# Kernel optimization log

Hardware: AMD Instinct MI355X
Metric: run time of the kernel (lower is better)

Reference implementation:

```python
import jax, jax.numpy as jnp
import numpy as np

B, T, D, SD, CHUNK = 4, 4096, 1024, 512, 32


def setup_inputs() -> dict:
    key = jax.random.key(0)
    ks = jax.random.split(key, 6)
    sc_in = 1.0 / np.sqrt(D)
    sc_out = 1.0 / np.sqrt(2 * SD)
    return {
        "x": jax.random.normal(ks[0], (B, T, D), jnp.float32),
        "Wt": jax.random.normal(ks[1], (D, SD), jnp.float32) * sc_in,
        "bt": jnp.zeros((SD,), jnp.float32),
        "Wr": jax.random.normal(ks[2], (D, SD), jnp.float32) * sc_in,
        "br": jnp.zeros((SD,), jnp.float32),
        "Wi": jax.random.normal(ks[3], (D, 2 * SD), jnp.float32) * sc_in,
        "bi": jnp.zeros((2 * SD,), jnp.float32),
        "Wo": jax.random.normal(ks[4], (2 * SD, D), jnp.float32) * sc_out,
        "bo": jnp.zeros((D,), jnp.float32),
        "gamma": jnp.ones((D,), jnp.float32),
        "beta": jnp.zeros((D,), jnp.float32),
    }


def _rotation_scan(theta, retain, b_r, b_i, chunk):
    # theta/retain/b_*: [B, T, d]. Chunked linear recurrence h[t]=a[t]*h[t-1]+b[t]
    # with a[t] = retain[t]*e^{i theta[t]}, done in log-magnitude/angle space.
    Bsz, Tlen, d = theta.shape
    K = min(chunk, Tlen)
    n = Tlen // K  # T assumed divisible by K (4096 / 32)
    resh = lambda a: a.reshape(Bsz, n, K, d).transpose(1, 0, 2, 3)  # [n,B,K,d]
    th_c, rt_c, br_c, bi_c = resh(theta), resh(retain), resh(b_r), resh(b_i)

    def step(carry, xs):
        h_r, h_i = carry  # [B, d]
        th, rt, cb_r, cb_i = xs  # [B, K, d]
        cum_log_mag = jnp.cumsum(jnp.log(jnp.clip(rt, 1e-6, None)), axis=1)
        cum_mag = jnp.exp(cum_log_mag)
        cum_th = jnp.cumsum(th, axis=1)
        cum_cos = jnp.cos(cum_th)
        cum_sin = jnp.sin(cum_th)
        cum_a_r = cum_mag * cum_cos
        cum_a_i = cum_mag * cum_sin
        inv_mag = 1.0 / jnp.clip(cum_mag, 1e-8, None)
        inv_r = inv_mag * cum_cos          # cos(-t) = cos(t)
        inv_i = -inv_mag * cum_sin         # sin(-t) = -sin(t)
        scaled_b_r = inv_r * cb_r - inv_i * cb_i
        scaled_b_i = inv_r * cb_i + inv_i * cb_r
        cum_b_r = jnp.cumsum(scaled_b_r, axis=1)
        cum_b_i = jnp.cumsum(scaled_b_i, axis=1)
        tot_r = h_r[:, None] + cum_b_r
        tot_i = h_i[:, None] + cum_b_i
        ch_r = cum_a_r * tot_r - cum_a_i * tot_i
        ch_i = cum_a_r * tot_i + cum_a_i * tot_r
        return (ch_r[:, -1], ch_i[:, -1]), (ch_r, ch_i)

    h0 = (jnp.zeros((Bsz, d), theta.dtype), jnp.zeros((Bsz, d), theta.dtype))
    _, (out_r, out_i) = jax.lax.scan(step, h0, (th_c, rt_c, br_c, bi_c))
    back = lambda a: a.transpose(1, 0, 2, 3).reshape(Bsz, Tlen, d)
    return back(out_r), back(out_i)


def reference(x, Wt, bt, Wr, br, Wi, bi, Wo, bo, gamma, beta):
    d = Wt.shape[1]
    theta = x @ Wt + bt                       # [B,T,d]
    retain = jax.nn.sigmoid(x @ Wr + br)      # [B,T,d]
    inp = x @ Wi + bi                          # [B,T,2d]
    inp_r, inp_i = inp[..., :d], inp[..., d:]
    drive = 1.0 - retain
    out_r, out_i = _rotation_scan(theta, retain, drive * inp_r, drive * inp_i, CHUNK)
    out = jnp.concatenate([out_r, out_i], axis=-1)  # [B,T,2d]
    y = x + out @ Wo + bo
    mu = jnp.mean(y, axis=-1, keepdims=True)
    var = jnp.var(y, axis=-1, keepdims=True)
    return (y - mu) / jnp.sqrt(var + 1e-5) * gamma + beta
```

## Files before the change

kernel.cpp:

```cpp
#include <hip/hip_runtime.h>
#include <cstdint>


typedef __bf16 bf16x8 __attribute__((ext_vector_type(8)));
typedef float  f32x4  __attribute__((ext_vector_type(4)));

#define AS1 __attribute__((address_space(1)))
#define AS3 __attribute__((address_space(3)))

__device__ __forceinline__ void gload16(const void* g, void* l) {
  __builtin_amdgcn_global_load_lds((const AS1 void*)g, (AS3 void*)l, 16, 0, 0);
}

__device__ __forceinline__ ushort f2bf(float f) {
  union { float f; uint32_t u; } v; v.f = f;
  uint32_t u = v.u;
  uint32_t r = u + 0x7FFFu + ((u >> 16) & 1u);
  return (ushort)(r >> 16);
}
__device__ __forceinline__ float bf2f(ushort u) {
  union { uint32_t x; float f; } v; v.x = (uint32_t)u << 16; return v.f;
}
__device__ __forceinline__ void st_f(float* p, size_t i, float v)  { p[i] = v; }
__device__ __forceinline__ void st_f(ushort* p, size_t i, float v) { p[i] = f2bf(v); }

__global__ __launch_bounds__(256) void tconv(const float* __restrict__ src, int R, int C,
                                             ushort* __restrict__ dst, int row_off) {
  __shared__ float tile[32][33];
  int tx = threadIdx.x, ty = threadIdx.y;
  int rb = blockIdx.y * 32, cb = blockIdx.x * 32;
#pragma unroll
  for (int yy = 0; yy < 4; ++yy) {
    int r = rb + ty + yy * 8;
    tile[ty + yy * 8][tx] = src[(size_t)r * C + cb + tx];
  }
  __syncthreads();
#pragma unroll
  for (int yy = 0; yy < 4; ++yy) {
    int c = cb + ty + yy * 8;
    dst[(size_t)(row_off + c) * R + rb + tx] = f2bf(tile[tx][ty + yy * 8]);
  }
}

__global__ __launch_bounds__(256) void pack_bias(const float* __restrict__ bt,
                                                 const float* __restrict__ br,
                                                 const float* __restrict__ bi,
                                                 float* __restrict__ bcat) {
  int i = blockIdx.x * 256 + threadIdx.x;
  bcat[i] = (i < 512) ? bt[i] : (i < 1024 ? br[i - 512] : bi[i - 1024]);
}

__global__ __launch_bounds__(256) void xconv(const float4* __restrict__ src,
                                             ushort* __restrict__ dst, int n4) {
  int i = blockIdx.x * 256 + threadIdx.x;
  if (i < n4) {
    float4 v = src[i];
    ushort4 o;
    o.x = f2bf(v.x); o.y = f2bf(v.y); o.z = f2bf(v.z); o.w = f2bf(v.w);
    *(ushort4*)(dst + (size_t)i * 4) = o;
  }
}

template <typename CT>
__global__ __launch_bounds__(512, 2) void gemm256(const ushort* __restrict__ A,
                                                  const ushort* __restrict__ Bt,
                                                  CT* __restrict__ C,
                                                  const float* __restrict__ bias,
                                                  int M, int N, int K, int nbn) {
  __shared__ alignas(16) ushort As[2][256 * 64];
  __shared__ alignas(16) ushort Bs[2][256 * 64];

  const int cpx = gridDim.x >> 3;
  const int wg = ((int)blockIdx.x & 7) * cpx + ((int)blockIdx.x >> 3);
  const int bm = wg / nbn, bn = wg % nbn;

  const int t = threadIdx.x;
  const int l = t & 63, w = t >> 6;
  const int wm = w >> 2, wn = w & 3;
  const int r = l & 15, kq = l >> 4;

  const size_t a0 = (size_t)bm * 256 * K;
  const size_t b0 = (size_t)bn * 256 * K;

  const int srow = t >> 3;
  const int sslot = (t & 7) ^ (srow & 7);
  const ushort* gA = A + a0 + (size_t)srow * K + sslot * 8;
  const ushort* gB = Bt + b0 + (size_t)srow * K + sslot * 8;
  const int lboff = w * 1024 + l * 16;

  f32x4 acc[8][4] = {};
  const int NKT = K >> 6;

#define STG(G, LB, kt, u) \
  gload16((G) + (size_t)((u) * 64) * K + (size_t)(kt) * 64, (char*)(LB) + (u) * 8192 + lboff)

#define QUAD(ph)                                                               \
  do {                                                                         \
    bf16x8 aF[2][2];                                                           \
    _Pragma("unroll")                                                          \
    for (int ii = 0; ii < 2; ++ii) {                                           \
      const int row = wm * 128 + ((ph) * 2 + ii) * 16 + r;                     \
      _Pragma("unroll")                                                        \
      for (int ks = 0; ks < 2; ++ks) {                                         \
        const int j = (ks * 4 + kq) ^ (r & 7);                                 \
        aF[ii][ks] = *(const bf16x8*)&As[cur][row * 64 + j * 8];               \
      }                                                                        \
    }                                                                          \
    __builtin_amdgcn_s_setprio(1);                                             \
    _Pragma("unroll")                                                          \
    for (int ii = 0; ii < 2; ++ii)                                             \
      _Pragma("unroll")                                                        \
      for (int jn = 0; jn < 4; ++jn)                                           \
        _Pragma("unroll")                                                      \
        for (int ks = 0; ks < 2; ++ks)                                         \
          acc[(ph) * 2 + ii][jn] = __builtin_amdgcn_mfma_f32_16x16x32_bf16(    \
              aF[ii][ks], bF[jn][ks], acc[(ph) * 2 + ii][jn], 0, 0, 0);        \
    __builtin_amdgcn_s_setprio(0);                                             \
  } while (0)

  STG(gB, Bs[0], 0, 0); STG(gB, Bs[0], 0, 1);
  STG(gB, Bs[0], 0, 2); STG(gB, Bs[0], 0, 3);
  STG(gA, As[0], 0, 0); STG(gA, As[0], 0, 2);
  STG(gA, As[0], 0, 1); STG(gA, As[0], 0, 3);

  for (int kt = 0; kt < NKT; ++kt) {
    const int cur = kt & 1, nxt = cur ^ 1;
    const bool hn = (kt + 1 < NKT);
    if (hn) { STG(gB, Bs[nxt], kt + 1, 0); STG(gB, Bs[nxt], kt + 1, 1); }
    if (hn) asm volatile("s_waitcnt vmcnt(4)" ::: "memory");
    else    asm volatile("s_waitcnt vmcnt(2)" ::: "memory");
    __builtin_amdgcn_s_barrier();
    asm volatile("" ::: "memory");
    bf16x8 bF[4][2];
#pragma unroll
    for (int jn = 0; jn < 4; ++jn) {
      const int row = wn * 64 + jn * 16 + r;
#pragma unroll
      for (int ks = 0; ks < 2; ++ks) {
        const int j = (ks * 4 + kq) ^ (r & 7);
        bF[jn][ks] = *(const bf16x8*)&Bs[cur][row * 64 + j * 8];
      }
    }
    QUAD(0);
    if (hn) { STG(gB, Bs[nxt], kt + 1, 2); STG(gB, Bs[nxt], kt + 1, 3); }
    QUAD(1);
    if (hn) { STG(gA, As[nxt], kt + 1, 0); STG(gA, As[nxt], kt + 1, 2); }
    if (hn) asm volatile("s_waitcnt vmcnt(6)" ::: "memory");
    else    asm volatile("s_waitcnt vmcnt(0)" ::: "memory");
    __builtin_amdgcn_s_barrier();
    asm volatile("" ::: "memory");
    QUAD(2);
    if (hn) { STG(gA, As[nxt], kt + 1, 1); STG(gA, As[nxt], kt + 1, 3); }
    QUAD(3);
  }
#undef STG
#undef QUAD

  const int q4 = (l >> 4) * 4;
#pragma unroll
  for (int i = 0; i < 8; ++i) {
#pragma unroll
    for (int jn = 0; jn < 4; ++jn) {
      const int gcol = bn * 256 + wn * 64 + jn * 16 + r;
      const float bv = bias ? bias[gcol] : 0.f;
#pragma unroll
      for (int q = 0; q < 4; ++q) {
        const int grow = bm * 256 + wm * 128 + i * 16 + q4 + q;
        st_f(C, (size_t)grow * N + gcol, acc[i][jn][q] + bv);
      }
    }
  }
}

__global__ __launch_bounds__(256) void scan_k1(const ushort* __restrict__ lin,
                                               float4* __restrict__ agg) {
  int bd = blockIdx.x * 256 + threadIdx.x;
  int c  = blockIdx.y;
  int b  = bd >> 9, d = bd & 511;
  const ushort* base = lin + ((size_t)b * 4096 + (size_t)c * 32) * 2048;
  float cth = 0.f, cbr = 0.f, cbi = 0.f;
  float cm = 1.f, cs = 1.f, sn = 0.f;
#pragma unroll 4
  for (int t = 0; t < 32; ++t) {
    const ushort* row = base + (size_t)t * 2048;
    float th = bf2f(row[d]);
    float z  = bf2f(row[512 + d]);
    float ir = bf2f(row[1024 + d]);
    float ii = bf2f(row[1536 + d]);
    float rt = __fdividef(1.f, 1.f + __expf(-z));
    cm *= fmaxf(rt, 1e-6f);
    cth += th;
    float s_, c_;
    __sincosf(cth, &s_, &c_);
    float im = __fdividef(1.f, fmaxf(cm, 1e-8f));
    float invr = im * c_, invi = -im * s_;
    float drive = 1.f - rt;
    float br_ = drive * ir, bi_ = drive * ii;
    cbr += invr * br_ - invi * bi_;
    cbi += invr * bi_ + invi * br_;
    cs = c_; sn = s_;
  }
  agg[(size_t)c * 2048 + bd] = make_float4(cm * cs, cm * sn, cbr, cbi);
}

__global__ __launch_bounds__(256) void scan_k2(const float4* __restrict__ agg,
                                               float2* __restrict__ h0) {
  int bd = blockIdx.x * 256 + threadIdx.x;
  float hr = 0.f, hi = 0.f;
  for (int cg = 0; cg < 16; ++cg) {
    float4 a[8];
#pragma unroll
    for (int u = 0; u < 8; ++u) a[u] = agg[(size_t)(cg * 8 + u) * 2048 + bd];
#pragma unroll
    for (int u = 0; u < 8; ++u) {
      h0[(size_t)(cg * 8 + u) * 2048 + bd] = make_float2(hr, hi);
      float tr = hr + a[u].z, ti = hi + a[u].w;
      hr = a[u].x * tr - a[u].y * ti;
      hi = a[u].x * ti + a[u].y * tr;
    }
  }
}

__global__ __launch_bounds__(256) void scan_k3(const ushort* __restrict__ lin,
                                               const float2* __restrict__ h0,
                                               ushort* __restrict__ outb) {
  int bd = blockIdx.x * 256 + threadIdx.x;
  int c  = blockIdx.y;
  int b  = bd >> 9, d = bd & 511;
  const ushort* base = lin + ((size_t)b * 4096 + (size_t)c * 32) * 2048;
  float2 h = h0[(size_t)c * 2048 + bd];
  float cth = 0.f, cbr = 0.f, cbi = 0.f, cm = 1.f;
#pragma unroll 4
  for (int t = 0; t < 32; ++t) {
    const ushort* row = base + (size_t)t * 2048;
    float th = bf2f(row[d]);
    float z  = bf2f(row[512 + d]);
    float ir = bf2f(row[1024 + d]);
    float ii = bf2f(row[1536 + d]);
    float rt = __fdividef(1.f, 1.f + __expf(-z));
    cm *= fmaxf(rt, 1e-6f);
    cth += th;
    float s_, c_;
    __sincosf(cth, &s_, &c_);
    float im = __fdividef(1.f, fmaxf(cm, 1e-8f));
    float invr = im * c_, invi = -im * s_;
    float drive = 1.f - rt;
    float br_ = drive * ir, bi_ = drive * ii;
    cbr += invr * br_ - invi * bi_;
    cbi += invr * bi_ + invi * br_;
    float ar = cm * c_, ai = cm * s_;
    float tr = h.x + cbr, ti = h.y + cbi;
    float orr = ar * tr - ai * ti;
    float oii = ar * ti + ai * tr;
    size_t rowo = ((size_t)b * 4096 + (size_t)c * 32 + t) * 1024;
    outb[rowo + d] = f2bf(orr);
    outb[rowo + 512 + d] = f2bf(oii);
  }
}

__global__ __launch_bounds__(256) void ln_k(const ushort* __restrict__ yb,
                                            const ushort* __restrict__ xb,
                                            const float* __restrict__ gamma,
                                            const float* __restrict__ beta,
                                            float* __restrict__ out) {
  int row = blockIdx.x;
  ushort4 uy = ((const ushort4*)(yb + (size_t)row * 1024))[threadIdx.x];
  ushort4 ux = ((const ushort4*)(xb + (size_t)row * 1024))[threadIdx.x];
  float4 v;
  v.x = bf2f(uy.x) + bf2f(ux.x);
  v.y = bf2f(uy.y) + bf2f(ux.y);
  v.z = bf2f(uy.z) + bf2f(ux.z);
  v.w = bf2f(uy.w) + bf2f(ux.w);
  float s  = v.x + v.y + v.z + v.w;
  float s2 = v.x * v.x + v.y * v.y + v.z * v.z + v.w * v.w;
#pragma unroll
  for (int off = 32; off > 0; off >>= 1) {
    s  += __shfl_down(s, off);
    s2 += __shfl_down(s2, off);
  }
  __shared__ float red[8];
  __shared__ float mv[2];
  int l = threadIdx.x & 63, w = threadIdx.x >> 6;
  if (l == 0) { red[w] = s; red[4 + w] = s2; }
  __syncthreads();
  if (threadIdx.x == 0) {
    float ts = red[0] + red[1] + red[2] + red[3];
    float t2 = red[4] + red[5] + red[6] + red[7];
    float mu = ts * (1.f / 1024.f);
    float var = t2 * (1.f / 1024.f) - mu * mu;
    mv[0] = mu;
    mv[1] = 1.f / sqrtf(var + 1e-5f);
  }
  __syncthreads();
  float mu = mv[0], rstd = mv[1];
  const float4* g4 = (const float4*)gamma;
  const float4* b4 = (const float4*)beta;
  float4 gv = g4[threadIdx.x], bv = b4[threadIdx.x];
  float4 o;
  o.x = (v.x - mu) * rstd * gv.x + bv.x;
  o.y = (v.y - mu) * rstd * gv.y + bv.y;
  o.z = (v.z - mu) * rstd * gv.z + bv.z;
  o.w = (v.w - mu) * rstd * gv.w + bv.w;
  ((float4*)(out + (size_t)row * 1024))[threadIdx.x] = o;
}

extern "C" void kernel_launch(void* const* d_in, const int* in_sizes, int n_in,
                              void* d_out, int out_size, void* d_ws, size_t ws_size,
                              hipStream_t stream) {
  (void)in_sizes; (void)n_in; (void)out_size; (void)ws_size;
  const float* x  = (const float*)d_in[0];
  const float* Wt = (const float*)d_in[1];
  const float* bt = (const float*)d_in[2];
  const float* Wr = (const float*)d_in[3];
  const float* br = (const float*)d_in[4];
  const float* Wi = (const float*)d_in[5];
  const float* bi = (const float*)d_in[6];
  const float* Wo = (const float*)d_in[7];
  const float* bo = (const float*)d_in[8];
  const float* gamma = (const float*)d_in[9];
  const float* beta  = (const float*)d_in[10];

  char* ws = (char*)d_ws;
  ushort* wcat_t = (ushort*)(ws);
  ushort* wo_t   = (ushort*)(ws + ((size_t)4  << 20));
  float*  bcat   = (float*) (ws + ((size_t)6  << 20));
  float4* agg    = (float4*)(ws + ((size_t)8  << 20));
  float2* h0     = (float2*)(ws + ((size_t)12 << 20));
  ushort* xb     = (ushort*)(ws + ((size_t)16 << 20));
  ushort* outb   = (ushort*)(ws + ((size_t)48 << 20));
  ushort* linb   = (ushort*)(ws + ((size_t)80 << 20));
  ushort* yb     = (ushort*)(ws + ((size_t)80 << 20));

  tconv<<<dim3(512 / 32, 1024 / 32), dim3(32, 8), 0, stream>>>(Wt, 1024, 512, wcat_t, 0);
  tconv<<<dim3(512 / 32, 1024 / 32), dim3(32, 8), 0, stream>>>(Wr, 1024, 512, wcat_t, 512);
  tconv<<<dim3(1024 / 32, 1024 / 32), dim3(32, 8), 0, stream>>>(Wi, 1024, 1024, wcat_t, 1024);
  tconv<<<dim3(1024 / 32, 1024 / 32), dim3(32, 8), 0, stream>>>(Wo, 1024, 1024, wo_t, 0);
  pack_bias<<<8, 256, 0, stream>>>(bt, br, bi, bcat);
  xconv<<<16384, 256, 0, stream>>>((const float4*)x, xb, 4194304);

  gemm256<ushort><<<512, 512, 0, stream>>>(
      xb, wcat_t, linb, bcat, 16384, 2048, 1024, 8);

  scan_k1<<<dim3(8, 128), 256, 0, stream>>>(linb, agg);
  scan_k2<<<8, 256, 0, stream>>>(agg, h0);
  scan_k3<<<dim3(8, 128), 256, 0, stream>>>(linb, h0, outb);

  gemm256<ushort><<<256, 512, 0, stream>>>(
      outb, wo_t, yb, bo, 16384, 1024, 1024, 4);

  ln_k<<<16384, 256, 0, stream>>>(yb, xb, gamma, beta, (float*)d_out);
}
```

Baseline: 228.7 us.

## Template GEMM tile height and stage epilogue through LDS for vector stores

The GEMM kernel gains a BM template parameter so the output projection runs with 128-row tiles and 512 workgroups instead of 256, which fills more CUs on the second GEMM. The epilogue now writes bf16 results into a swizzled LDS tile and then issues 16-byte coalesced global stores, replacing scattered 2-byte stores. This adds an extra barrier and LDS round trip at the end of each tile, and the smaller tile lowers reuse of the B operand.

```diff
diff --git a/kernel.cpp b/kernel.cpp
--- a/kernel.cpp
+++ b/kernel.cpp
@@ -4,6 +4,7 @@
 
 typedef __bf16 bf16x8 __attribute__((ext_vector_type(8)));
 typedef float  f32x4  __attribute__((ext_vector_type(4)));
+typedef ushort u16x8  __attribute__((ext_vector_type(8)));
 
 #define AS1 __attribute__((address_space(1)))
 #define AS3 __attribute__((address_space(3)))
@@ -21,8 +22,6 @@
 __device__ __forceinline__ float bf2f(ushort u) {
   union { uint32_t x; float f; } v; v.x = (uint32_t)u << 16; return v.f;
 }
-__device__ __forceinline__ void st_f(float* p, size_t i, float v)  { p[i] = v; }
-__device__ __forceinline__ void st_f(ushort* p, size_t i, float v) { p[i] = f2bf(v); }
 
 __global__ __launch_bounds__(256) void tconv(const float* __restrict__ src, int R, int C,
                                              ushort* __restrict__ dst, int row_off) {
@@ -61,14 +60,20 @@
   }
 }
 
-template <typename CT>
+template <int BM>
 __global__ __launch_bounds__(512, 2) void gemm256(const ushort* __restrict__ A,
                                                   const ushort* __restrict__ Bt,
-                                                  CT* __restrict__ C,
+                                                  ushort* __restrict__ C,
                                                   const float* __restrict__ bias,
                                                   int M, int N, int K, int nbn) {
-  __shared__ alignas(16) ushort As[2][256 * 64];
-  __shared__ alignas(16) ushort Bs[2][256 * 64];
+  constexpr int MI = BM / 32;
+  constexpr int II = BM / 128;
+  constexpr int STAGE_USH = 2 * (BM * 64 + 256 * 64);
+  constexpr int CT_USH = BM * 256;
+  constexpr int SM_USH = (STAGE_USH > CT_USH) ? STAGE_USH : CT_USH;
+  __shared__ alignas(16) ushort smem[SM_USH];
+  ushort* const As0 = smem;
+  ushort* const Bs0 = smem + 2 * BM * 64;
 
   const int cpx = gridDim.x >> 3;
   const int wg = ((int)blockIdx.x & 7) * cpx + ((int)blockIdx.x >> 3);
@@ -79,7 +84,7 @@
   const int wm = w >> 2, wn = w & 3;
   const int r = l & 15, kq = l >> 4;
 
-  const size_t a0 = (size_t)bm * 256 * K;
+  const size_t a0 = (size_t)bm * BM * K;
   const size_t b0 = (size_t)bn * 256 * K;
 
   const int srow = t >> 3;
@@ -88,87 +93,126 @@
   const ushort* gB = Bt + b0 + (size_t)srow * K + sslot * 8;
   const int lboff = w * 1024 + l * 16;
 
-  f32x4 acc[8][4] = {};
+  f32x4 acc[MI][4] = {};
   const int NKT = K >> 6;
 
-#define STG(G, LB, kt, u) \
-  gload16((G) + (size_t)((u) * 64) * K + (size_t)(kt) * 64, (char*)(LB) + (u) * 8192 + lboff)
+#define STGA(buf, kt, u) \
+  gload16(gA + (size_t)((u) * 64) * K + (size_t)(kt) * 64, \
+          (char*)(As0 + (buf) * BM * 64) + (u) * 8192 + lboff)
+#define STGB(buf, kt, u) \
+  gload16(gB + (size_t)((u) * 64) * K + (size_t)(kt) * 64, \
+          (char*)(Bs0 + (buf) * 256 * 64) + (u) * 8192 + lboff)
 
 #define QUAD(ph)                                                               \
   do {                                                                         \
-    bf16x8 aF[2][2];                                                           \
     _Pragma("unroll")                                                          \
-    for (int ii = 0; ii < 2; ++ii) {                                           \
-      const int row = wm * 128 + ((ph) * 2 + ii) * 16 + r;                     \
+    for (int ii = 0; ii < II; ++ii) {                                          \
+      bf16x8 aF[2];                                                            \
+      const int rowa = wm * (BM / 2) + ((ph) * II + ii) * 16 + r;              \
       _Pragma("unroll")                                                        \
       for (int ks = 0; ks < 2; ++ks) {                                         \
         const int j = (ks * 4 + kq) ^ (r & 7);                                 \
-        aF[ii][ks] = *(const bf16x8*)&As[cur][row * 64 + j * 8];               \
+        aF[ks] = *(const bf16x8*)&pA[rowa * 64 + j * 8];                       \
       }                                                                        \
-    }                                                                          \
-    __builtin_amdgcn_s_setprio(1);                                             \
-    _Pragma("unroll")                                                          \
-    for (int ii = 0; ii < 2; ++ii)                                             \
+      __builtin_amdgcn_s_setprio(1);                                           \
       _Pragma("unroll")                                                        \
       for (int jn = 0; jn < 4; ++jn)                                           \
         _Pragma("unroll")                                                      \
         for (int ks = 0; ks < 2; ++ks)                                         \
-          acc[(ph) * 2 + ii][jn] = __builtin_amdgcn_mfma_f32_16x16x32_bf16(    \
-              aF[ii][ks], bF[jn][ks], acc[(ph) * 2 + ii][jn], 0, 0, 0);        \
-    __builtin_amdgcn_s_setprio(0);                                             \
+          acc[(ph) * II + ii][jn] = __builtin_amdgcn_mfma_f32_16x16x32_bf16(   \
+              aF[ks], bF[jn][ks], acc[(ph) * II + ii][jn], 0, 0, 0);           \
+      __builtin_amdgcn_s_setprio(0);                                           \
+    }                                                                          \
   } while (0)
 
-  STG(gB, Bs[0], 0, 0); STG(gB, Bs[0], 0, 1);
-  STG(gB, Bs[0], 0, 2); STG(gB, Bs[0], 0, 3);
-  STG(gA, As[0], 0, 0); STG(gA, As[0], 0, 2);
-  STG(gA, As[0], 0, 1); STG(gA, As[0], 0, 3);
+  STGB(0, 0, 0); STGB(0, 0, 1); STGB(0, 0, 2); STGB(0, 0, 3);
+  if constexpr (BM == 256) { STGA(0, 0, 0); STGA(0, 0, 2); STGA(0, 0, 1); STGA(0, 0, 3); }
+  else                     { STGA(0, 0, 0); STGA(0, 0, 1); }
 
   for (int kt = 0; kt < NKT; ++kt) {
     const int cur = kt & 1, nxt = cur ^ 1;
     const bool hn = (kt + 1 < NKT);
-    if (hn) { STG(gB, Bs[nxt], kt + 1, 0); STG(gB, Bs[nxt], kt + 1, 1); }
-    if (hn) asm volatile("s_waitcnt vmcnt(4)" ::: "memory");
-    else    asm volatile("s_waitcnt vmcnt(2)" ::: "memory");
+    const ushort* pA = As0 + cur * BM * 64;
+    const ushort* pB = Bs0 + cur * 256 * 64;
+    if (hn) { STGB(nxt, kt + 1, 0); STGB(nxt, kt + 1, 1); }
+    if constexpr (BM == 256) {
+      if (hn) asm volatile("s_waitcnt vmcnt(4)" ::: "memory");
+      else    asm volatile("s_waitcnt vmcnt(2)" ::: "memory");
+    } else {
+      if (hn) asm volatile("s_waitcnt vmcnt(2)" ::: "memory");
+      else    asm volatile("s_waitcnt vmcnt(0)" ::: "memory");
+    }
     __builtin_amdgcn_s_barrier();
     asm volatile("" ::: "memory");
     bf16x8 bF[4][2];
 #pragma unroll
     for (int jn = 0; jn < 4; ++jn) {
-      const int row = wn * 64 + jn * 16 + r;
+      const int rowb = wn * 64 + jn * 16 + r;
 #pragma unroll
       for (int ks = 0; ks < 2; ++ks) {
         const int j = (ks * 4 + kq) ^ (r & 7);
-        bF[jn][ks] = *(const bf16x8*)&Bs[cur][row * 64 + j * 8];
+        bF[jn][ks] = *(const bf16x8*)&pB[rowb * 64 + j * 8];
       }
     }
     QUAD(0);
-    if (hn) { STG(gB, Bs[nxt], kt + 1, 2); STG(gB, Bs[nxt], kt + 1, 3); }
+    if (hn) { STGB(nxt, kt + 1, 2); STGB(nxt, kt + 1, 3); }
     QUAD(1);
-    if (hn) { STG(gA, As[nxt], kt + 1, 0); STG(gA, As[nxt], kt + 1, 2); }
-    if (hn) asm volatile("s_waitcnt vmcnt(6)" ::: "memory");
-    else    asm volatile("s_waitcnt vmcnt(0)" ::: "memory");
+    if (hn) {
+      if constexpr (BM == 256) { STGA(nxt, kt + 1, 0); STGA(nxt, kt + 1, 2); }
+      else                     { STGA(nxt, kt + 1, 0); }
+    }
+    if constexpr (BM == 256) {
+      if (hn) asm volatile("s_waitcnt vmcnt(6)" ::: "memory");
+      else    asm volatile("s_waitcnt vmcnt(0)" ::: "memory");
+    }
     __builtin_amdgcn_s_barrier();
     asm volatile("" ::: "memory");
     QUAD(2);
-    if (hn) { STG(gA, As[nxt], kt + 1, 1); STG(gA, As[nxt], kt + 1, 3); }
+    if (hn) {
+      if constexpr (BM == 256) { STGA(nxt, kt + 1, 1); STGA(nxt, kt + 1, 3); }
+      else                     { STGA(nxt, kt + 1, 1); }
+    }
     QUAD(3);
   }
-#undef STG
+#undef STGA
+#undef STGB
 #undef QUAD
 
+  asm volatile("s_waitcnt lgkmcnt(0) vmcnt(0)" ::: "memory");
+  __builtin_amdgcn_s_barrier();
+
   const int q4 = (l >> 4) * 4;
-#pragma unroll
-  for (int i = 0; i < 8; ++i) {
+  float bvj[4];
+#pragma unroll
+  for (int jn = 0; jn < 4; ++jn) {
+    const int col = wn * 64 + jn * 16 + r;
+    bvj[jn] = bias ? bias[bn * 256 + col] : 0.f;
+  }
+#pragma unroll
+  for (int i = 0; i < MI; ++i) {
 #pragma unroll
     for (int jn = 0; jn < 4; ++jn) {
-      const int gcol = bn * 256 + wn * 64 + jn * 16 + r;
-      const float bv = bias ? bias[gcol] : 0.f;
+      const int col = wn * 64 + jn * 16 + r;
+      const int chunk = col >> 3;
 #pragma unroll
       for (int q = 0; q < 4; ++q) {
-        const int grow = bm * 256 + wm * 128 + i * 16 + q4 + q;
-        st_f(C, (size_t)grow * N + gcol, acc[i][jn][q] + bv);
+        const int rowl = wm * (BM / 2) + i * 16 + q4 + q;
+        const int pch = chunk ^ (rowl & 7);
+        smem[rowl * 256 + pch * 8 + (col & 7)] = f2bf(acc[i][jn][q] + bvj[jn]);
       }
     }
+  }
+  __builtin_amdgcn_s_barrier();
+
+  const int rrow0 = t >> 5;
+  const int rch = t & 31;
+#pragma unroll
+  for (int p = 0; p < BM / 16; ++p) {
+    const int rowl = p * 16 + rrow0;
+    const int pch = rch ^ (rowl & 7);
+    u16x8 vv = *(const u16x8*)&smem[rowl * 256 + pch * 8];
+    const size_t grow = (size_t)(bm * BM + rowl);
+    *(u16x8*)&C[grow * N + bn * 256 + rch * 8] = vv;
   }
 }
 
@@ -338,15 +382,13 @@
   pack_bias<<<8, 256, 0, stream>>>(bt, br, bi, bcat);
   xconv<<<16384, 256, 0, stream>>>((const float4*)x, xb, 4194304);
 
-  gemm256<ushort><<<512, 512, 0, stream>>>(
-      xb, wcat_t, linb, bcat, 16384, 2048, 1024, 8);
+  gemm256<256><<<512, 512, 0, stream>>>(xb, wcat_t, linb, bcat, 16384, 2048, 1024, 8);
 
   scan_k1<<<dim3(8, 128), 256, 0, stream>>>(linb, agg);
   scan_k2<<<8, 256, 0, stream>>>(agg, h0);
   scan_k3<<<dim3(8, 128), 256, 0, stream>>>(linb, h0, outb);
 
-  gemm256<ushort><<<256, 512, 0, stream>>>(
-      outb, wo_t, yb, bo, 16384, 1024, 1024, 4);
+  gemm256<128><<<512, 512, 0, stream>>>(outb, wo_t, yb, bo, 16384, 1024, 1024, 4);
 
   ln_k<<<16384, 256, 0, stream>>>(yb, xb, gamma, beta, (float*)d_out);
 }
```

Result: faster. 213.3 us (-6.7%).
